# Optimization experiments

Hardware: AMD Instinct MI355X
Metric: run time of the kernel (lower is better)

## Reference

```python
import jax, jax.numpy as jnp
import numpy as np

B, USER_DIM, ITEM_DIM, LATENT = 8192, 3706, 6040, 512


def setup_inputs() -> dict:
    key = jax.random.key(0)
    kx, kwu, kwi = jax.random.split(key, 3)
    scale_u = 1.0 / np.sqrt(USER_DIM)
    scale_i = 1.0 / np.sqrt(ITEM_DIM)
    return {
        "x": jax.random.normal(kx, (B, USER_DIM + ITEM_DIM), dtype=jnp.float32),
        "Wu": jax.random.normal(kwu, (LATENT, USER_DIM), dtype=jnp.float32) * scale_u,
        "bu": jnp.zeros((LATENT,), dtype=jnp.float32),
        "Wi": jax.random.normal(kwi, (LATENT, ITEM_DIM), dtype=jnp.float32) * scale_i,
        "bi": jnp.zeros((LATENT,), dtype=jnp.float32),
    }


def reference(x, Wu, bu, Wi, bi):
    # mDA encode: linear + relu for each tower
    user_emb = jax.nn.relu(x[:, :USER_DIM] @ Wu.T + bu)   # [B, LATENT]
    item_emb = jax.nn.relu(x[:, -ITEM_DIM:] @ Wi.T + bi)  # [B, LATENT]
    # torch.mm(u, i.T).diag() == row-wise dot product (same math, O(B*d) not O(B^2*d))
    diag = jnp.einsum("bd,bd->b", user_emb, item_emb)     # [B]
    return diag[:, None]                                   # [B, 1]
```

## Files before the change

kernel.cpp:

```cpp
#include <hip/hip_runtime.h>
#include <hip/hip_bf16.h>
#include <stdint.h>

#define USER_DIM 3706
#define ITEM_DIM 6040
#define LATENT   512
#define BATCH    8192
#define XCOLS    (USER_DIM + ITEM_DIM)
#define KPAD_U   3712
#define KPAD_I   6144

typedef float f32x4 __attribute__((ext_vector_type(4)));
typedef short bf16x8 __attribute__((ext_vector_type(8)));

#define VMCNT(n) asm volatile("s_waitcnt vmcnt(" #n ")" ::: "memory")

static __device__ __forceinline__ unsigned short f2bf(float f) {
    union { float f; unsigned int u; } v; v.f = f;
    unsigned int u = v.u;
    u += 0x7fffu + ((u >> 16) & 1u);
    return (unsigned short)(u >> 16);
}
static __device__ __forceinline__ float bf2f(unsigned int b) {
    union { unsigned int u; float f; } v; v.u = b << 16; return v.f;
}
static __device__ __forceinline__ short cvt1(float f) {
    union { __hip_bfloat16 h; unsigned short u; } cv;
    cv.h = __float2bfloat16(f);
    return (short)cv.u;
}
static __device__ __forceinline__ bf16x8 cvt8(f32x4 lo, f32x4 hi) {
    bf16x8 r;
    #pragma unroll
    for (int i = 0; i < 4; ++i) { r[i] = cvt1(lo[i]); r[4 + i] = cvt1(hi[i]); }
    return r;
}
static __device__ __forceinline__ void gload16(const void* g, void* l) {
    __builtin_amdgcn_global_load_lds(
        (const __attribute__((address_space(1))) void*)g,
        (__attribute__((address_space(3))) void*)l, 16, 0, 0);
}
static __device__ __forceinline__ void BARRIER() {
    __builtin_amdgcn_sched_barrier(0);
    __builtin_amdgcn_s_barrier();
    __builtin_amdgcn_sched_barrier(0);
}

__global__ void convert_w(const float* __restrict__ W, unsigned short* __restrict__ Wb,
                          int K, int Kpad) {
    int c = blockIdx.x * blockDim.x + threadIdx.x;
    int r = blockIdx.y;
    if (c >= Kpad) return;
    unsigned short o = 0;
    if (c < K) o = f2bf(W[(size_t)r * K + c]);
    Wb[(size_t)r * Kpad + c] = o;
}

__global__ __launch_bounds__(256, 3) void gemm_fused(
    const float* __restrict__ X,
    const unsigned short* __restrict__ WuB, const float* __restrict__ bu,
    const unsigned short* __restrict__ WiB,
    unsigned short* __restrict__ Uemb,
    unsigned short* __restrict__ P0, unsigned short* __restrict__ P1)
{
    __shared__ float          sA2[2][128 * 32];
    __shared__ unsigned short sB2[2][128 * 32];

    const int tid  = threadIdx.x;
    const int lane = tid & 63;
    const int wid  = tid >> 6;
    const int wm   = wid >> 1;
    const int wn   = wid & 1;

    const int bid = blockIdx.x;
    const int swz = (bid & 7) * 96 + (bid >> 3);
    const int g4  = swz >> 2;
    const int nb  = swz & 3;

    int mb, k0, nt, xoff, Kpad;
    const unsigned short* WB;
    bool isUser; int kh = 0;
    if (g4 % 3 == 0) {
        isUser = true;  mb = g4 / 3;
        k0 = 0; nt = KPAD_U / 32; xoff = 0; Kpad = KPAD_U; WB = WuB;
    } else {
        const int q = g4 - (g4 / 3 + 1);
        isUser = false; mb = q >> 1; kh = q & 1;
        k0 = kh * 96; nt = 96; xoff = USER_DIM; Kpad = KPAD_I; WB = WiB;
    }

    const int a_ri = lane >> 3;
    const int a_cs = (lane & 7) ^ a_ri;
    const int b_si = lane >> 3;
    const int b_c8 = (lane & 7) ^ b_si;
    const int b_rr = b_c8 >> 2;
    const int b_cc = b_c8 & 3;

    auto ISSUE = [&](int t, int buf) {
        const int kb = t * 32;
        float*          sA = sA2[buf];
        unsigned short* sB = sB2[buf];
        #pragma unroll
        for (int j = 0; j < 4; ++j) {
            const int i   = wid * 4 + j;
            const int row = mb * 128 + i * 8 + a_ri;
            const int xc  = xoff + kb + a_cs * 4;
            const float* s = X + (size_t)row * XCOLS + xc;
            if (xc + 4 > XCOLS) s = X;
            gload16(s, sA + i * 256);
        }
        #pragma unroll
        for (int j = 0; j < 2; ++j) {
            const int i  = wid * 2 + j;
            const int rt = (i * 8 + b_si) * 2 + b_rr;
            const unsigned short* s =
                WB + (size_t)(nb * 128 + rt) * Kpad + kb + b_cc * 8;
            gload16(s, sB + i * 512);
        }
    };

    const int fr = lane & 15;
    const int g  = lane >> 4;

    f32x4 acc[4][4];
    #pragma unroll
    for (int i = 0; i < 4; ++i)
        #pragma unroll
        for (int j = 0; j < 4; ++j) acc[i][j] = (f32x4)0.0f;

    auto COMPUTE = [&](int buf) {
        const float*          sA = sA2[buf];
        const unsigned short* sB = sB2[buf];
        bf16x8 af[4], bfr[4];
        #pragma unroll
        for (int mi = 0; mi < 4; ++mi) {
            const int r = wm * 64 + mi * 16 + fr;
            const float* base = sA + r * 32;
            const int s = r & 7;
            f32x4 lo = *(const f32x4*)(base + (((2 * g)     ^ s) * 4));
            f32x4 hi = *(const f32x4*)(base + (((2 * g + 1) ^ s) * 4));
            af[mi] = cvt8(lo, hi);
        }
        #pragma unroll
        for (int ni = 0; ni < 4; ++ni) {
            const int r   = wn * 64 + ni * 16 + fr;
            const int seg = r >> 1;
            const int c8  = ((r & 1) * 4 + g) ^ (seg & 7);
            bfr[ni] = *(const bf16x8*)(sB + seg * 64 + c8 * 8);
        }
        #pragma unroll
        for (int mi = 0; mi < 4; ++mi)
            #pragma unroll
            for (int ni = 0; ni < 4; ++ni)
                acc[mi][ni] = __builtin_amdgcn_mfma_f32_16x16x32_bf16(
                    af[mi], bfr[ni], acc[mi][ni], 0, 0, 0);
    };

    ISSUE(k0, 0);
    VMCNT(0);
    BARRIER();
    ISSUE(k0 + 1, 1);

    for (int t = 0; t < nt; ++t) {
        COMPUTE(t & 1);
        BARRIER();
        if (t + 2 < nt) {
            ISSUE(k0 + t + 2, t & 1);
            VMCNT(6);
        } else {
            VMCNT(0);
        }
        BARRIER();
    }

    const int cb = nb * 128 + wn * 64;
    const int rb = mb * 128 + wm * 64 + (lane >> 4) * 4;
    if (isUser) {
        #pragma unroll
        for (int ni = 0; ni < 4; ++ni) {
            const int col = cb + ni * 16 + fr;
            const float bv = bu[col];
            #pragma unroll
            for (int mi = 0; mi < 4; ++mi) {
                f32x4 v = acc[mi][ni];
                #pragma unroll
                for (int r = 0; r < 4; ++r) {
                    const int row = rb + mi * 16 + r;
                    Uemb[(size_t)row * LATENT + col] = f2bf(fmaxf(v[r] + bv, 0.0f));
                }
            }
        }
    } else {
        unsigned short* P = kh ? P1 : P0;
        #pragma unroll
        for (int ni = 0; ni < 4; ++ni) {
            const int col = cb + ni * 16 + fr;
            #pragma unroll
            for (int mi = 0; mi < 4; ++mi) {
                f32x4 v = acc[mi][ni];
                #pragma unroll
                for (int r = 0; r < 4; ++r) {
                    const int row = rb + mi * 16 + r;
                    P[(size_t)row * LATENT + col] = f2bf(v[r]);
                }
            }
        }
    }
}

__global__ void rowdot(const unsigned short* __restrict__ U,
                       const unsigned short* __restrict__ P0,
                       const unsigned short* __restrict__ P1,
                       const float* __restrict__ bi,
                       float* __restrict__ out) {
    const int lane = threadIdx.x & 63;
    const int w    = threadIdx.x >> 6;
    const int row  = blockIdx.x * 4 + w;
    const size_t base = (size_t)row * LATENT + lane * 8;
    const uint4 uv = *(const uint4*)(U  + base);
    const uint4 p0 = *(const uint4*)(P0 + base);
    const uint4 p1 = *(const uint4*)(P1 + base);
    const float4 b0 = *(const float4*)(bi + lane * 8);
    const float4 b1 = *(const float4*)(bi + lane * 8 + 4);
    const float bb[8] = {b0.x, b0.y, b0.z, b0.w, b1.x, b1.y, b1.z, b1.w};
    const unsigned int* up = (const unsigned int*)&uv;
    const unsigned int* q0 = (const unsigned int*)&p0;
    const unsigned int* q1 = (const unsigned int*)&p1;
    float acc = 0.0f;
    #pragma unroll
    for (int q = 0; q < 4; ++q) {
        float ilo = fmaxf(bf2f(q0[q] & 0xffffu) + bf2f(q1[q] & 0xffffu) + bb[2 * q], 0.0f);
        float ihi = fmaxf(bf2f(q0[q] >> 16)     + bf2f(q1[q] >> 16)     + bb[2 * q + 1], 0.0f);
        acc += bf2f(up[q] & 0xffffu) * ilo;
        acc += bf2f(up[q] >> 16)     * ihi;
    }
    #pragma unroll
    for (int off = 32; off >= 1; off >>= 1)
        acc += __shfl_xor(acc, off, 64);
    if (lane == 0) out[row] = acc;
}

extern "C" void kernel_launch(void* const* d_in, const int* in_sizes, int n_in,
                              void* d_out, int out_size, void* d_ws, size_t ws_size,
                              hipStream_t stream) {
    const float* x  = (const float*)d_in[0];
    const float* Wu = (const float*)d_in[1];
    const float* bu = (const float*)d_in[2];
    const float* Wi = (const float*)d_in[3];
    const float* bi = (const float*)d_in[4];
    float* out = (float*)d_out;

    unsigned short* WuB  = (unsigned short*)d_ws;
    unsigned short* WiB  = WuB + (size_t)LATENT * KPAD_U;
    unsigned short* Uemb = WiB + (size_t)LATENT * KPAD_I;
    unsigned short* P0   = Uemb + (size_t)BATCH * LATENT;
    unsigned short* P1   = P0   + (size_t)BATCH * LATENT;

    convert_w<<<dim3((KPAD_U + 255) / 256, LATENT), 256, 0, stream>>>(Wu, WuB, USER_DIM, KPAD_U);
    convert_w<<<dim3((KPAD_I + 255) / 256, LATENT), 256, 0, stream>>>(Wi, WiB, ITEM_DIM, KPAD_I);

    gemm_fused<<<768, 256, 0, stream>>>(x, WuB, bu, WiB, Uemb, P0, P1);

    rowdot<<<BATCH / 4, 256, 0, stream>>>(Uemb, P0, P1, bi, out);
}
```

Baseline: 237.1 us.

## Convert X tiles to bf16 once in registers before LDS staging

The A operand was staged in LDS as fp32 and converted to bf16 for every MFMA fragment read. Now each thread loads X into registers, converts once, and writes packed bf16 into LDS. This halves A's LDS footprint and removes the repeated conversions from the compute loop. The loop is restructured so the global load for the next tile overlaps compute, with adjusted waitcnts, setprio around the MFMAs, and a peeled final iteration. The risks are extra register pressure and synchronous global loads replacing async direct-to-LDS loads.

After: 222.6 us. 6.1% less time.

```diff
diff --git a/kernel.cpp b/kernel.cpp
--- a/kernel.cpp
+++ b/kernel.cpp
@@ -14,6 +14,7 @@
 typedef short bf16x8 __attribute__((ext_vector_type(8)));
 
 #define VMCNT(n) asm volatile("s_waitcnt vmcnt(" #n ")" ::: "memory")
+#define LGKM0    asm volatile("s_waitcnt lgkmcnt(0)" ::: "memory")
 
 static __device__ __forceinline__ unsigned short f2bf(float f) {
     union { float f; unsigned int u; } v; v.f = f;
@@ -23,17 +24,6 @@
 }
 static __device__ __forceinline__ float bf2f(unsigned int b) {
     union { unsigned int u; float f; } v; v.u = b << 16; return v.f;
-}
-static __device__ __forceinline__ short cvt1(float f) {
-    union { __hip_bfloat16 h; unsigned short u; } cv;
-    cv.h = __float2bfloat16(f);
-    return (short)cv.u;
-}
-static __device__ __forceinline__ bf16x8 cvt8(f32x4 lo, f32x4 hi) {
-    bf16x8 r;
-    #pragma unroll
-    for (int i = 0; i < 4; ++i) { r[i] = cvt1(lo[i]); r[4 + i] = cvt1(hi[i]); }
-    return r;
 }
 static __device__ __forceinline__ void gload16(const void* g, void* l) {
     __builtin_amdgcn_global_load_lds(
@@ -63,8 +53,8 @@
     unsigned short* __restrict__ Uemb,
     unsigned short* __restrict__ P0, unsigned short* __restrict__ P1)
 {
-    __shared__ float          sA2[2][128 * 32];
-    __shared__ unsigned short sB2[2][128 * 32];
+    __shared__ unsigned short sA2[2][64 * 64];
+    __shared__ unsigned short sB2[2][64 * 64];
 
     const int tid  = threadIdx.x;
     const int lane = tid & 63;
@@ -89,38 +79,58 @@
         k0 = kh * 96; nt = 96; xoff = USER_DIM; Kpad = KPAD_I; WB = WiB;
     }
 
-    const int a_ri = lane >> 3;
-    const int a_cs = (lane & 7) ^ a_ri;
-    const int b_si = lane >> 3;
-    const int b_c8 = (lane & 7) ^ b_si;
-    const int b_rr = b_c8 >> 2;
-    const int b_cc = b_c8 & 3;
-
-    auto ISSUE = [&](int t, int buf) {
+    const int l8  = lane >> 3;
+    const int c8w = lane & 7;
+    const int s8  = c8w ^ l8;
+    const int spr = s8 >> 2;
+    const int skc = (s8 & 3) * 8;
+
+    float4 raf[2][2];
+
+    auto ALOAD = [&](int t) {
         const int kb = t * 32;
-        float*          sA = sA2[buf];
+        #pragma unroll
+        for (int o = 0; o < 2; ++o) {
+            const int sego = wid * 16 + o * 8 + l8;
+            const int grow = mb * 128 + sego * 2 + spr;
+            const int xc   = xoff + kb + skc;
+            const float* s = X + (size_t)grow * XCOLS + xc;
+            if (xc + 8 > XCOLS) s = X;
+            raf[o][0] = *(const float4*)s;
+            raf[o][1] = *(const float4*)(s + 4);
+        }
+    };
+    auto AWRITE = [&](int buf) {
+        unsigned short* sA = sA2[buf];
+        #pragma unroll
+        for (int o = 0; o < 2; ++o) {
+            const int sego = wid * 16 + o * 8 + l8;
+            uint4 w;
+            w.x = (unsigned)f2bf(raf[o][0].x) | ((unsigned)f2bf(raf[o][0].y) << 16);
+            w.y = (unsigned)f2bf(raf[o][0].z) | ((unsigned)f2bf(raf[o][0].w) << 16);
+            w.z = (unsigned)f2bf(raf[o][1].x) | ((unsigned)f2bf(raf[o][1].y) << 16);
+            w.w = (unsigned)f2bf(raf[o][1].z) | ((unsigned)f2bf(raf[o][1].w) << 16);
+            *(uint4*)(sA + sego * 64 + c8w * 8) = w;
+        }
+    };
+    auto ISSUE_B = [&](int t, int buf) {
+        const int kb = t * 32;
         unsigned short* sB = sB2[buf];
-        #pragma unroll
-        for (int j = 0; j < 4; ++j) {
-            const int i   = wid * 4 + j;
-            const int row = mb * 128 + i * 8 + a_ri;
-            const int xc  = xoff + kb + a_cs * 4;
-            const float* s = X + (size_t)row * XCOLS + xc;
-            if (xc + 4 > XCOLS) s = X;
-            gload16(s, sA + i * 256);
-        }
         #pragma unroll
         for (int j = 0; j < 2; ++j) {
             const int i  = wid * 2 + j;
-            const int rt = (i * 8 + b_si) * 2 + b_rr;
+            const int rt = (i * 8 + l8) * 2 + spr;
             const unsigned short* s =
-                WB + (size_t)(nb * 128 + rt) * Kpad + kb + b_cc * 8;
+                WB + (size_t)(nb * 128 + rt) * Kpad + kb + skc;
             gload16(s, sB + i * 512);
         }
     };
 
-    const int fr = lane & 15;
-    const int g  = lane >> 4;
+    const int fr   = lane & 15;
+    const int g    = lane >> 4;
+    const int rc8  = ((((fr & 1) * 4) + g) ^ (fr >> 1)) * 8;
+    const int aro  = (wm * 32 + (fr >> 1)) * 64 + rc8;
+    const int bro  = (wn * 32 + (fr >> 1)) * 64 + rc8;
 
     f32x4 acc[4][4];
     #pragma unroll
@@ -129,49 +139,53 @@
         for (int j = 0; j < 4; ++j) acc[i][j] = (f32x4)0.0f;
 
     auto COMPUTE = [&](int buf) {
-        const float*          sA = sA2[buf];
+        const unsigned short* sA = sA2[buf];
         const unsigned short* sB = sB2[buf];
         bf16x8 af[4], bfr[4];
         #pragma unroll
-        for (int mi = 0; mi < 4; ++mi) {
-            const int r = wm * 64 + mi * 16 + fr;
-            const float* base = sA + r * 32;
-            const int s = r & 7;
-            f32x4 lo = *(const f32x4*)(base + (((2 * g)     ^ s) * 4));
-            f32x4 hi = *(const f32x4*)(base + (((2 * g + 1) ^ s) * 4));
-            af[mi] = cvt8(lo, hi);
-        }
-        #pragma unroll
-        for (int ni = 0; ni < 4; ++ni) {
-            const int r   = wn * 64 + ni * 16 + fr;
-            const int seg = r >> 1;
-            const int c8  = ((r & 1) * 4 + g) ^ (seg & 7);
-            bfr[ni] = *(const bf16x8*)(sB + seg * 64 + c8 * 8);
-        }
+        for (int mi = 0; mi < 4; ++mi)
+            af[mi] = *(const bf16x8*)(sA + aro + mi * 512);
+        #pragma unroll
+        for (int ni = 0; ni < 4; ++ni)
+            bfr[ni] = *(const bf16x8*)(sB + bro + ni * 512);
+        __builtin_amdgcn_s_setprio(1);
         #pragma unroll
         for (int mi = 0; mi < 4; ++mi)
             #pragma unroll
             for (int ni = 0; ni < 4; ++ni)
                 acc[mi][ni] = __builtin_amdgcn_mfma_f32_16x16x32_bf16(
                     af[mi], bfr[ni], acc[mi][ni], 0, 0, 0);
-    };
-
-    ISSUE(k0, 0);
+        __builtin_amdgcn_s_setprio(0);
+    };
+
+    ALOAD(k0);
+    ISSUE_B(k0, 0);
+    AWRITE(0);
+    ALOAD(k0 + 1);
+    LGKM0;
+    VMCNT(4);
+    BARRIER();
+    ISSUE_B(k0 + 1, 1);
+
+    #pragma unroll 2
+    for (int t = 0; t < nt - 2; ++t) {
+        const int cur = t & 1;
+        COMPUTE(cur);
+        AWRITE(cur ^ 1);
+        ALOAD(k0 + t + 2);
+        LGKM0;
+        BARRIER();
+        ISSUE_B(k0 + t + 2, cur);
+        VMCNT(6);
+        BARRIER();
+    }
+    COMPUTE(0);
+    AWRITE(1);
+    LGKM0;
+    BARRIER();
     VMCNT(0);
     BARRIER();
-    ISSUE(k0 + 1, 1);
-
-    for (int t = 0; t < nt; ++t) {
-        COMPUTE(t & 1);
-        BARRIER();
-        if (t + 2 < nt) {
-            ISSUE(k0 + t + 2, t & 1);
-            VMCNT(6);
-        } else {
-            VMCNT(0);
-        }
-        BARRIER();
-    }
+    COMPUTE(1);
 
     const int cb = nb * 128 + wn * 64;
     const int rb = mb * 128 + wm * 64 + (lane >> 4) * 4;
```
